# Performance work log

Hardware: AMD Instinct MI355X
Metric: run time of the kernel (lower is better)

## Reference

```python
import jax, jax.numpy as jnp
import numpy as np
from jax import lax


def _dw(x, w):
    # x: (C,H,W), w: (C,1,kh,kw) -> depthwise 'same' conv, groups=C
    return lax.conv_general_dilated(
        x[None], w, window_strides=(1, 1), padding='SAME',
        dimension_numbers=('NCHW', 'OIHW', 'NCHW'),
        feature_group_count=x.shape[0])[0]

_dw_b = jax.vmap(_dw)  # per-batch-element dynamic depthwise conv


def setup_inputs() -> dict:
    key = jax.random.key(0)
    ks = jax.random.split(key, 6)
    Q, B, C, H, W = 100, 8, 64, 256, 256
    return {
        'query': jax.random.normal(ks[0], (Q, B, C), jnp.float32),
        'value': jax.random.normal(ks[1], (B, C, H, W), jnp.float32),
        'hard_sigmoid_masks': jnp.zeros((1,), jnp.float32),
        'pos2': jnp.zeros((1,), jnp.float32),
        'pos3': jnp.zeros((1,), jnp.float32),
        'Wl': jax.random.normal(ks[2], (18, 100), jnp.float32) * 0.1,
        'bl': jax.random.normal(ks[3], (18,), jnp.float32) * 0.1,
        'Wd': jax.random.normal(ks[4], (100, 18), jnp.float32) * 0.1,
        'bd': jax.random.normal(ks[5], (100,), jnp.float32) * 0.1,
    }


def reference(query, value, hard_sigmoid_masks, pos2, pos3, Wl, bl, Wd, bd):
    Qn, B, C = query.shape
    # weight_linear on query.permute(1,2,0): (B,C,100) @ Wl.T + bl -> (B,C,18)
    conv1d = jnp.einsum('qbc,kq->bck', query, Wl) + bl
    former = conv1d[..., :9].reshape(B, C, 1, 3, 3)   # filt1
    wk = conv1d[..., 9:].reshape(B, C, 1, 3, 3)        # weight_conv1d

    y_temp = _dw_b(value, former)                       # (B,C,H,W)
    diff = jnp.exp(-(value - y_temp) ** 2)
    filt2 = lax.stop_gradient(jnp.abs(wk))
    y_diff9 = _dw_b(diff, filt2)
    vd = value * diff
    res = _dw_b(vd, wk)
    weights_d = wk.sum(axis=(2, 3), keepdims=True)      # (B,C,1,1,3) -> 1x3 kernel
    res_diff = _dw_b(vd, weights_d)
    y_diff = (res - res_diff) / (y_diff9 + 1e-10)
    y = y_temp - y_diff

    weight1 = jnp.concatenate([former.reshape(B, C, 9), wk.reshape(B, C, 9)], axis=-1)
    q = jnp.einsum('bck,nk->bcn', weight1, Wd) + bd     # (B,C,100)
    return (q.transpose(2, 0, 1), y)
```

## Files before the change

kernel.cpp:

```cpp
#include <hip/hip_runtime.h>
#include <math.h>

#define HH 256
#define WW 256
#define BC 512
#define QN 100

__global__ __launch_bounds__(128) void prep_kernel(
    const float* __restrict__ query,
    const float* __restrict__ Wl,
    const float* __restrict__ bl,
    const float* __restrict__ Wd,
    const float* __restrict__ bd,
    float* __restrict__ qout,
    float* __restrict__ coef)
{
    const int bc = blockIdx.x;
    const int t  = threadIdx.x;
    __shared__ float qcol[QN];
    __shared__ float c18[18];

    if (t < QN) qcol[t] = query[t * BC + bc];
    __syncthreads();

    if (t < 18) {
        float acc = bl[t];
        const float* wrow = Wl + t * QN;
        #pragma unroll 4
        for (int qi = 0; qi < QN; ++qi) acc += qcol[qi] * wrow[qi];
        c18[t] = acc;
    }
    __syncthreads();

    if (t < QN) {
        float acc = bd[t];
        const float* wrow = Wd + t * 18;
        #pragma unroll
        for (int k = 0; k < 18; ++k) acc += c18[k] * wrow[k];
        qout[t * BC + bc] = acc;
    }

    if (t < 18) {
        coef[bc * 32 + t] = c18[t];
    } else if (t < 27) {
        coef[bc * 32 + t] = fabsf(c18[t - 9]);
    } else if (t < 30) {
        int j = t - 27;
        coef[bc * 32 + t] = c18[9 + j] + c18[12 + j] + c18[15 + j];
    }
}

__global__ __launch_bounds__(256) void fused_kernel(
    const float* __restrict__ value,
    const float* __restrict__ coef,
    float* __restrict__ yout)
{
    const int bc = blockIdx.z;
    const int h0 = blockIdx.y * 32;
    const int w0 = blockIdx.x * 32;
    const int tid = threadIdx.x;

    __shared__ float sval[36][37];
    __shared__ float sdiff[34][36];
    __shared__ float syt[34][36];
    __shared__ float sc[32];

    if (tid < 30) sc[tid] = coef[bc * 32 + tid];

    const float* vp = value + (size_t)bc * (HH * WW);

    #pragma unroll
    for (int it = 0; it < 6; ++it) {
        int idx = tid + it * 256;
        if (idx < 36 * 36) {
            int r = idx / 36, c = idx - r * 36;
            int h = h0 - 2 + r, w = w0 - 2 + c;
            float v = 0.f;
            if ((unsigned)h < HH && (unsigned)w < WW) v = vp[h * WW + w];
            sval[r][c] = v;
        }
    }
    __syncthreads();

    float f[9];
    #pragma unroll
    for (int i = 0; i < 9; ++i) f[i] = sc[i];

    #pragma unroll
    for (int it = 0; it < 5; ++it) {
        int idx = tid + it * 256;
        if (idx < 34 * 34) {
            int r = idx / 34, c = idx - r * 34;
            float yt = 0.f;
            #pragma unroll
            for (int i = 0; i < 3; ++i)
                #pragma unroll
                for (int j = 0; j < 3; ++j)
                    yt += f[i * 3 + j] * sval[r + i][c + j];
            float v = sval[r + 1][c + 1];
            float e = v - yt;
            float d = __expf(-e * e);
            int h = h0 - 1 + r, w = w0 - 1 + c;
            if ((unsigned)h >= HH || (unsigned)w >= WW) d = 0.f;
            sdiff[r][c] = d;
            syt[r][c]   = yt;
        }
    }
    __syncthreads();

    float wk[9], awk[9], wsum[3];
    #pragma unroll
    for (int i = 0; i < 9; ++i) { wk[i] = sc[9 + i]; awk[i] = sc[18 + i]; }
    #pragma unroll
    for (int j = 0; j < 3; ++j) wsum[j] = sc[27 + j];

    const int r  = tid >> 3;
    const int c0 = (tid & 7) * 4;

    float dreg[3][6], vreg[3][6];
    #pragma unroll
    for (int i = 0; i < 3; ++i)
        #pragma unroll
        for (int j = 0; j < 6; ++j) {
            dreg[i][j] = sdiff[r + i][c0 + j];
            vreg[i][j] = sval[r + 1 + i][c0 + 1 + j];
        }

    float4 outv;
    float* outp = &outv.x;
    #pragma unroll
    for (int p = 0; p < 4; ++p) {
        float yd9 = 1e-10f;
        float rs  = 0.f;
        #pragma unroll
        for (int i = 0; i < 3; ++i)
            #pragma unroll
            for (int j = 0; j < 3; ++j) {
                float dd = dreg[i][p + j];
                yd9 += dd * awk[i * 3 + j];
                rs  += dd * vreg[i][p + j] * wk[i * 3 + j];
            }
        float rd = 0.f;
        #pragma unroll
        for (int j = 0; j < 3; ++j)
            rd += dreg[1][p + j] * vreg[1][p + j] * wsum[j];
        float yt = syt[r + 1][c0 + 1 + p];
        outp[p] = yt - (rs - rd) / yd9;
    }

    float* dst = yout + (size_t)bc * (HH * WW) + (size_t)(h0 + r) * WW + (w0 + c0);
    *reinterpret_cast<float4*>(dst) = outv;
}

extern "C" void kernel_launch(void* const* d_in, const int* in_sizes, int n_in,
                              void* d_out, int out_size, void* d_ws, size_t ws_size,
                              hipStream_t stream) {
    const float* query = (const float*)d_in[0];
    const float* value = (const float*)d_in[1];
    const float* Wl    = (const float*)d_in[5];
    const float* bl    = (const float*)d_in[6];
    const float* Wd    = (const float*)d_in[7];
    const float* bd    = (const float*)d_in[8];

    float* out   = (float*)d_out;
    float* qout  = out;
    float* yout  = out + QN * BC;
    float* coef  = (float*)d_ws;

    prep_kernel<<<BC, 128, 0, stream>>>(query, Wl, bl, Wd, bd, qout, coef);

    dim3 grid(WW / 32, HH / 32, BC);
    fused_kernel<<<grid, 256, 0, stream>>>(value, coef, yout);
}
```

Before: 321.3 us.

## Register-block first stencil pass, drop syt buffer, vectorize LDS reads

Restructures the fused depthwise stencil kernel. Each thread now computes the first 3x3 conv and diff for a 4-wide strip, using float4 LDS loads into registers, and a separate small branch fills the 2-wide halo. The y_temp shared buffer is dropped and y_temp is recomputed in the second pass, and coefficients are read straight from global into registers. The aim is to cut scalar LDS traffic, integer div/mod indexing and shared memory footprint. The cost is extra FMAs, higher register pressure, and possible LDS bank conflicts now that sval has no row padding.

```diff
diff --git a/kernel.cpp b/kernel.cpp
--- a/kernel.cpp
+++ b/kernel.cpp
@@ -50,6 +50,12 @@
     }
 }
 
+#define LD8(dst, ptr0) { \
+    float4 _x = *(const float4*)(ptr0); \
+    float4 _y = *(const float4*)((ptr0) + 4); \
+    dst[0]=_x.x; dst[1]=_x.y; dst[2]=_x.z; dst[3]=_x.w; \
+    dst[4]=_y.x; dst[5]=_y.y; dst[6]=_y.z; dst[7]=_y.w; }
+
 __global__ __launch_bounds__(256) void fused_kernel(
     const float* __restrict__ value,
     const float* __restrict__ coef,
@@ -60,12 +66,14 @@
     const int w0 = blockIdx.x * 32;
     const int tid = threadIdx.x;
 
-    __shared__ float sval[36][37];
-    __shared__ float sdiff[34][36];
-    __shared__ float syt[34][36];
-    __shared__ float sc[32];
+    __shared__ __align__(16) float sval[36][36];
+    __shared__ __align__(16) float sdiff[34][36];
 
-    if (tid < 30) sc[tid] = coef[bc * 32 + tid];
+    const float* cp = coef + bc * 32;
+    float fco[9], wk[9], awk[9], ws[3];
+    #pragma unroll
+    for (int i = 0; i < 9; ++i) { fco[i] = cp[i]; wk[i] = cp[9 + i]; awk[i] = cp[18 + i]; }
+    ws[0] = cp[27]; ws[1] = cp[28]; ws[2] = cp[29];
 
     const float* vp = value + (size_t)bc * (HH * WW);
 
@@ -82,74 +90,91 @@
     }
     __syncthreads();
 
-    float f[9];
-    #pragma unroll
-    for (int i = 0; i < 9; ++i) f[i] = sc[i];
+    const int r  = tid >> 3;
+    const int c0 = (tid & 7) << 2;
 
-    #pragma unroll
-    for (int it = 0; it < 5; ++it) {
-        int idx = tid + it * 256;
-        if (idx < 34 * 34) {
-            int r = idx / 34, c = idx - r * 34;
+    {
+        float b0[8], b1[8], b2[8];
+        LD8(b0, &sval[r][c0]);
+        LD8(b1, &sval[r + 1][c0]);
+        LD8(b2, &sval[r + 2][c0]);
+
+        float4 dq;
+        float* dd = &dq.x;
+        #pragma unroll
+        for (int p = 0; p < 4; ++p) {
             float yt = 0.f;
             #pragma unroll
-            for (int i = 0; i < 3; ++i)
-                #pragma unroll
-                for (int j = 0; j < 3; ++j)
-                    yt += f[i * 3 + j] * sval[r + i][c + j];
-            float v = sval[r + 1][c + 1];
+            for (int j = 0; j < 3; ++j)
+                yt += fco[j] * b0[p + j] + fco[3 + j] * b1[p + j] + fco[6 + j] * b2[p + j];
+            float v = b1[p + 1];
             float e = v - yt;
             float d = __expf(-e * e);
-            int h = h0 - 1 + r, w = w0 - 1 + c;
+            int h = h0 - 1 + r, w = w0 - 1 + c0 + p;
             if ((unsigned)h >= HH || (unsigned)w >= WW) d = 0.f;
-            sdiff[r][c] = d;
-            syt[r][c]   = yt;
+            dd[p] = d;
         }
+        *(float4*)&sdiff[r][c0] = dq;
+    }
+
+    if (tid < 132) {
+        int rr, cc;
+        if (tid < 68) { rr = 32 + (tid >= 34 ? 1 : 0); cc = tid - (tid >= 34 ? 34 : 0); }
+        else          { int ee = tid - 68; rr = ee >> 1; cc = 32 + (ee & 1); }
+        float yt = 0.f;
+        #pragma unroll
+        for (int i = 0; i < 3; ++i)
+            #pragma unroll
+            for (int j = 0; j < 3; ++j)
+                yt += fco[i * 3 + j] * sval[rr + i][cc + j];
+        float v = sval[rr + 1][cc + 1];
+        float e = v - yt;
+        float d = __expf(-e * e);
+        int h = h0 - 1 + rr, w = w0 - 1 + cc;
+        if ((unsigned)h >= HH || (unsigned)w >= WW) d = 0.f;
+        sdiff[rr][cc] = d;
     }
     __syncthreads();
 
-    float wk[9], awk[9], wsum[3];
-    #pragma unroll
-    for (int i = 0; i < 9; ++i) { wk[i] = sc[9 + i]; awk[i] = sc[18 + i]; }
-    #pragma unroll
-    for (int j = 0; j < 3; ++j) wsum[j] = sc[27 + j];
+    {
+        float a0[8], a1[8], a2[8];
+        float q0[8], q1[8], q2[8];
+        LD8(a0, &sdiff[r][c0]);
+        LD8(a1, &sdiff[r + 1][c0]);
+        LD8(a2, &sdiff[r + 2][c0]);
+        LD8(q0, &sval[r + 1][c0]);
+        LD8(q1, &sval[r + 2][c0]);
+        LD8(q2, &sval[r + 3][c0]);
 
-    const int r  = tid >> 3;
-    const int c0 = (tid & 7) * 4;
-
-    float dreg[3][6], vreg[3][6];
-    #pragma unroll
-    for (int i = 0; i < 3; ++i)
+        float pd0[6], pd1[6], pd2[6];
         #pragma unroll
         for (int j = 0; j < 6; ++j) {
-            dreg[i][j] = sdiff[r + i][c0 + j];
-            vreg[i][j] = sval[r + 1 + i][c0 + 1 + j];
+            pd0[j] = a0[j] * q0[j + 1];
+            pd1[j] = a1[j] * q1[j + 1];
+            pd2[j] = a2[j] * q2[j + 1];
         }
 
-    float4 outv;
-    float* outp = &outv.x;
-    #pragma unroll
-    for (int p = 0; p < 4; ++p) {
-        float yd9 = 1e-10f;
-        float rs  = 0.f;
+        float4 outv;
+        float* outp = &outv.x;
         #pragma unroll
-        for (int i = 0; i < 3; ++i)
+        for (int p = 0; p < 4; ++p) {
+            float yt  = 0.f;
+            float yd9 = 1e-10f;
+            float rs  = 0.f;
+            float rd  = 0.f;
             #pragma unroll
             for (int j = 0; j < 3; ++j) {
-                float dd = dreg[i][p + j];
-                yd9 += dd * awk[i * 3 + j];
-                rs  += dd * vreg[i][p + j] * wk[i * 3 + j];
+                yt  += fco[j] * q0[p + 1 + j] + fco[3 + j] * q1[p + 1 + j] + fco[6 + j] * q2[p + 1 + j];
+                yd9 += awk[j] * a0[p + j]     + awk[3 + j] * a1[p + j]     + awk[6 + j] * a2[p + j];
+                rs  += wk[j]  * pd0[p + j]    + wk[3 + j]  * pd1[p + j]    + wk[6 + j]  * pd2[p + j];
+                rd  += ws[j]  * pd1[p + j];
             }
-        float rd = 0.f;
-        #pragma unroll
-        for (int j = 0; j < 3; ++j)
-            rd += dreg[1][p + j] * vreg[1][p + j] * wsum[j];
-        float yt = syt[r + 1][c0 + 1 + p];
-        outp[p] = yt - (rs - rd) / yd9;
+            outp[p] = yt - (rs - rd) / yd9;
+        }
+
+        float* dst = yout + (size_t)bc * (HH * WW) + (size_t)(h0 + r) * WW + (w0 + c0);
+        *reinterpret_cast<float4*>(dst) = outv;
     }
-
-    float* dst = yout + (size_t)bc * (HH * WW) + (size_t)(h0 + r) * WW + (w0 + c0);
-    *reinterpret_cast<float4*>(dst) = outv;
 }
 
 extern "C" void kernel_launch(void* const* d_in, const int* in_sizes, int n_in,
```

Result: no change. 321.1 us (-0.1%).

## Use 64x64 tiles with row-sliding register windows and recompute y_temp

Applied to the files above, without the earlier changes.

Enlarges each block's tile from 32x32 to 64x64 to cut halo overhead, and loads the value tile with float2 accesses. Each wave sweeps down columns, keeping 3x3 windows in registers that slide row by row. The syt shared buffer is dropped: y_temp is recomputed in the final pass from sval. The division becomes a fast reciprocal, and output is written as scalar coalesced rows instead of float4. The cost is more shared memory per block (about 36KB), which lowers occupancy, plus fewer blocks, a slight precision change from rcp, and redundant y_temp arithmetic.

```diff
diff --git a/kernel.cpp b/kernel.cpp
--- a/kernel.cpp
+++ b/kernel.cpp
@@ -55,101 +55,125 @@
     const float* __restrict__ coef,
     float* __restrict__ yout)
 {
-    const int bc = blockIdx.z;
-    const int h0 = blockIdx.y * 32;
-    const int w0 = blockIdx.x * 32;
+    const int bc  = blockIdx.z;
+    const int h0  = blockIdx.y * 64;
+    const int w0  = blockIdx.x * 64;
     const int tid = threadIdx.x;
+    const int wave = tid >> 6;
+    const int lane = tid & 63;
 
-    __shared__ float sval[36][37];
-    __shared__ float sdiff[34][36];
-    __shared__ float syt[34][36];
-    __shared__ float sc[32];
+    __shared__ __align__(16) float sval[68][68];
+    __shared__ __align__(16) float sdiff[66][68];
 
-    if (tid < 30) sc[tid] = coef[bc * 32 + tid];
+    const float* cp = coef + bc * 32;
+    float fco[9], wk[9], awk[9], ws[3];
+    #pragma unroll
+    for (int i = 0; i < 9; ++i) { fco[i] = cp[i]; wk[i] = cp[9 + i]; awk[i] = cp[18 + i]; }
+    ws[0] = cp[27]; ws[1] = cp[28]; ws[2] = cp[29];
 
     const float* vp = value + (size_t)bc * (HH * WW);
 
     #pragma unroll
-    for (int it = 0; it < 6; ++it) {
+    for (int it = 0; it < 10; ++it) {
         int idx = tid + it * 256;
-        if (idx < 36 * 36) {
-            int r = idx / 36, c = idx - r * 36;
-            int h = h0 - 2 + r, w = w0 - 2 + c;
-            float v = 0.f;
-            if ((unsigned)h < HH && (unsigned)w < WW) v = vp[h * WW + w];
-            sval[r][c] = v;
+        if (idx < 68 * 34) {
+            int r = idx / 34;
+            int m = idx - r * 34;
+            int h = h0 - 2 + r;
+            int w = w0 - 2 + 2 * m;
+            float2 v = make_float2(0.f, 0.f);
+            if ((unsigned)h < HH) {
+                const float* rowp = vp + h * WW;
+                if ((unsigned)w < WW)       v.x = rowp[w];
+                if ((unsigned)(w + 1) < WW) v.y = rowp[w + 1];
+            }
+            *(float2*)&sval[r][2 * m] = v;
         }
     }
     __syncthreads();
 
-    float f[9];
-    #pragma unroll
-    for (int i = 0; i < 9; ++i) f[i] = sc[i];
+    {
+        const int lo = (wave < 2) ? 17 * wave : 34 + 16 * (wave - 2);
+        const int hi = (wave < 2) ? lo + 17 : lo + 16;
+        const int x  = lane;
+        float t00 = sval[lo][x],     t01 = sval[lo][x + 1],     t02 = sval[lo][x + 2];
+        float t10 = sval[lo + 1][x], t11 = sval[lo + 1][x + 1], t12 = sval[lo + 1][x + 2];
+        for (int r = lo; r < hi; ++r) {
+            float t20 = sval[r + 2][x], t21 = sval[r + 2][x + 1], t22 = sval[r + 2][x + 2];
+            float yt = fco[0]*t00 + fco[1]*t01 + fco[2]*t02
+                     + fco[3]*t10 + fco[4]*t11 + fco[5]*t12
+                     + fco[6]*t20 + fco[7]*t21 + fco[8]*t22;
+            float e = t11 - yt;
+            float d = __expf(-e * e);
+            if ((unsigned)(h0 - 1 + r) >= HH || (unsigned)(w0 - 1 + x) >= WW) d = 0.f;
+            sdiff[r][x] = d;
+            t00 = t10; t01 = t11; t02 = t12;
+            t10 = t20; t11 = t21; t12 = t22;
+        }
+    }
 
-    #pragma unroll
-    for (int it = 0; it < 5; ++it) {
-        int idx = tid + it * 256;
-        if (idx < 34 * 34) {
-            int r = idx / 34, c = idx - r * 34;
-            float yt = 0.f;
+    if (tid < 132) {
+        int r = tid >> 1;
+        int c = 64 + (tid & 1);
+        float yt = 0.f;
+        #pragma unroll
+        for (int u = 0; u < 3; ++u)
             #pragma unroll
-            for (int i = 0; i < 3; ++i)
-                #pragma unroll
-                for (int j = 0; j < 3; ++j)
-                    yt += f[i * 3 + j] * sval[r + i][c + j];
-            float v = sval[r + 1][c + 1];
-            float e = v - yt;
-            float d = __expf(-e * e);
-            int h = h0 - 1 + r, w = w0 - 1 + c;
-            if ((unsigned)h >= HH || (unsigned)w >= WW) d = 0.f;
-            sdiff[r][c] = d;
-            syt[r][c]   = yt;
-        }
+            for (int v = 0; v < 3; ++v)
+                yt += fco[u * 3 + v] * sval[r + u][c + v];
+        float e = sval[r + 1][c + 1] - yt;
+        float d = __expf(-e * e);
+        if ((unsigned)(h0 - 1 + r) >= HH || (unsigned)(w0 - 1 + c) >= WW) d = 0.f;
+        sdiff[r][c] = d;
     }
     __syncthreads();
 
-    float wk[9], awk[9], wsum[3];
-    #pragma unroll
-    for (int i = 0; i < 9; ++i) { wk[i] = sc[9 + i]; awk[i] = sc[18 + i]; }
-    #pragma unroll
-    for (int j = 0; j < 3; ++j) wsum[j] = sc[27 + j];
+    {
+        const int y0 = wave * 16;
+        const int x  = lane;
+        float* dst = yout + (size_t)bc * (HH * WW) + (size_t)(h0 + y0) * WW + (w0 + x);
 
-    const int r  = tid >> 3;
-    const int c0 = (tid & 7) * 4;
-
-    float dreg[3][6], vreg[3][6];
-    #pragma unroll
-    for (int i = 0; i < 3; ++i)
+        float sd0[3], sd1[3], sd2[3];
+        float sv0[3], sv1[3], sv2[3];
+        float vd0[3], vd1[3], vd2[3];
         #pragma unroll
-        for (int j = 0; j < 6; ++j) {
-            dreg[i][j] = sdiff[r + i][c0 + j];
-            vreg[i][j] = sval[r + 1 + i][c0 + 1 + j];
+        for (int b = 0; b < 3; ++b) {
+            sd0[b] = sdiff[y0][x + b];
+            sv0[b] = sval[y0 + 1][x + 1 + b];
+            vd0[b] = sd0[b] * sv0[b];
+            sd1[b] = sdiff[y0 + 1][x + b];
+            sv1[b] = sval[y0 + 2][x + 1 + b];
+            vd1[b] = sd1[b] * sv1[b];
         }
-
-    float4 outv;
-    float* outp = &outv.x;
-    #pragma unroll
-    for (int p = 0; p < 4; ++p) {
-        float yd9 = 1e-10f;
-        float rs  = 0.f;
         #pragma unroll
-        for (int i = 0; i < 3; ++i)
+        for (int i = 0; i < 16; ++i) {
+            const int y = y0 + i;
             #pragma unroll
-            for (int j = 0; j < 3; ++j) {
-                float dd = dreg[i][p + j];
-                yd9 += dd * awk[i * 3 + j];
-                rs  += dd * vreg[i][p + j] * wk[i * 3 + j];
+            for (int b = 0; b < 3; ++b) {
+                sd2[b] = sdiff[y + 2][x + b];
+                sv2[b] = sval[y + 3][x + 1 + b];
+                vd2[b] = sd2[b] * sv2[b];
             }
-        float rd = 0.f;
-        #pragma unroll
-        for (int j = 0; j < 3; ++j)
-            rd += dreg[1][p + j] * vreg[1][p + j] * wsum[j];
-        float yt = syt[r + 1][c0 + 1 + p];
-        outp[p] = yt - (rs - rd) / yd9;
+            float yt  = fco[0]*sv0[0] + fco[1]*sv0[1] + fco[2]*sv0[2]
+                      + fco[3]*sv1[0] + fco[4]*sv1[1] + fco[5]*sv1[2]
+                      + fco[6]*sv2[0] + fco[7]*sv2[1] + fco[8]*sv2[2];
+            float yd9 = 1e-10f
+                      + awk[0]*sd0[0] + awk[1]*sd0[1] + awk[2]*sd0[2]
+                      + awk[3]*sd1[0] + awk[4]*sd1[1] + awk[5]*sd1[2]
+                      + awk[6]*sd2[0] + awk[7]*sd2[1] + awk[8]*sd2[2];
+            float rs  = wk[0]*vd0[0] + wk[1]*vd0[1] + wk[2]*vd0[2]
+                      + wk[3]*vd1[0] + wk[4]*vd1[1] + wk[5]*vd1[2]
+                      + wk[6]*vd2[0] + wk[7]*vd2[1] + wk[8]*vd2[2];
+            float rd  = ws[0]*vd1[0] + ws[1]*vd1[1] + ws[2]*vd1[2];
+            float inv = __builtin_amdgcn_rcpf(yd9);
+            dst[i * WW] = yt - (rs - rd) * inv;
+            #pragma unroll
+            for (int b = 0; b < 3; ++b) {
+                sd0[b] = sd1[b]; sv0[b] = sv1[b]; vd0[b] = vd1[b];
+                sd1[b] = sd2[b]; sv1[b] = sv2[b]; vd1[b] = vd2[b];
+            }
+        }
     }
-
-    float* dst = yout + (size_t)bc * (HH * WW) + (size_t)(h0 + r) * WW + (w0 + c0);
-    *reinterpret_cast<float4*>(dst) = outv;
 }
 
 extern "C" void kernel_launch(void* const* d_in, const int* in_sizes, int n_in,
@@ -169,6 +193,6 @@
 
     prep_kernel<<<BC, 128, 0, stream>>>(query, Wl, bl, Wd, bd, qout, coef);
 
-    dim3 grid(WW / 32, HH / 32, BC);
+    dim3 grid(WW / 64, HH / 64, BC);
     fused_kernel<<<grid, 256, 0, stream>>>(value, coef, yout);
 }
```

Result: faster. 309.6 us (-3.6%).
